# Kernel tuning notes

Measured on AMD Instinct MI355X. Metric: run time of the kernel, lower is better.

## Reference

```python
import jax, jax.numpy as jnp
import numpy as np

N_NODES = 50000
N_EDGES = 1_600_000
IN_CH = 128
HEADS = 4
OUT_CH = 16
NEG_SLOPE = 0.2


def setup_inputs() -> dict:
    key = jax.random.key(0)
    ks = jax.random.split(key, 6)
    x = jax.random.normal(ks[0], (N_NODES, IN_CH), dtype=jnp.float32)
    row = jax.random.randint(ks[1], (N_EDGES,), 0, N_NODES, dtype=jnp.int32)
    # offset in [1, N) guarantees no self loops in the input graph
    off = jax.random.randint(ks[2], (N_EDGES,), 1, N_NODES, dtype=jnp.int32)
    col = (row + off) % N_NODES
    edge_index = jnp.stack([row, col], axis=0)  # [2, E]
    edge_attr = jax.random.uniform(ks[3], (N_EDGES, HEADS), dtype=jnp.float32)
    weight = jax.random.normal(ks[4], (IN_CH, HEADS * OUT_CH), dtype=jnp.float32) * (1.0 / np.sqrt(IN_CH))
    att_weight = jax.random.normal(ks[5], (1, HEADS, 2 * OUT_CH), dtype=jnp.float32) * 0.1
    bias = jnp.zeros((HEADS * OUT_CH,), dtype=jnp.float32)
    return {"x": x, "edge_index": edge_index, "edge_attr": edge_attr,
            "weight": weight, "att_weight": att_weight, "bias": bias}


def reference(x, edge_index, edge_attr, weight, att_weight, bias):
    N = x.shape[0]
    H, C = HEADS, OUT_CH
    # linear projection: [N, in] @ [in, H*C] -> [N, H, C]
    h = (x @ weight).reshape(N, H, C)
    # add self loops (input is guaranteed self-loop free); self-loop edge_attr = 1
    loop = jnp.arange(N, dtype=edge_index.dtype)
    row = jnp.concatenate([edge_index[0], loop])
    col = jnp.concatenate([edge_index[1], loop])
    ea = jnp.concatenate([edge_attr, jnp.ones((N, H), dtype=edge_attr.dtype)], axis=0)
    edge_index_full = jnp.stack([row, col], axis=0)
    # attention score: cat([h[row], h[col]], -1) * att_weight, summed over feature dim
    a_src = att_weight[0, :, :C]   # [H, C]
    a_dst = att_weight[0, :, C:]   # [H, C]
    alpha = (jnp.einsum('ehc,hc->eh', h[row], a_src)
             + jnp.einsum('ehc,hc->eh', h[col], a_dst))  # [E+N, H]
    alpha = jnp.where(alpha >= 0, alpha, NEG_SLOPE * alpha)  # leaky_relu
    alpha = alpha * ea
    # weighted aggregation: scatter-add messages to row nodes
    msg = alpha[:, :, None] * h[col]                 # [E+N, H, C]
    out = jax.ops.segment_sum(msg, row, num_segments=N)  # [N, H, C]
    out = out.reshape(N, H * C) + bias               # concat heads
    return (out, edge_index_full, alpha)
```

## Files before the change

kernel.cpp:

```cpp
#include <hip/hip_runtime.h>

#define N_NODES 50000
#define N_EDGES 1600000
#define IN_CH 128
#define HEADS 4
#define HC 64
#define E_FULL (N_EDGES + N_NODES)
#define NEG_SLOPE 0.2f

#define BUCKET_NODES 98
#define NBUCK 512
#define BIN_TILE 2048
#define NBLK_BIN ((N_EDGES + BIN_TILE - 1) / BIN_TILE)
#define T_FLAT (NBUCK * NBLK_BIN)
#define SCANA_BLOCKS (T_FLAT / 256)

typedef __attribute__((ext_vector_type(8))) short short8v;
typedef __attribute__((ext_vector_type(4))) float float4v;

__device__ __forceinline__ float leaky(float s) { return s >= 0.f ? s : NEG_SLOPE * s; }

__device__ __forceinline__ unsigned f2bf(float f) {
    unsigned u = __float_as_uint(f);
    return (u + 0x7fffu + ((u >> 16) & 1u)) >> 16;
}
__device__ __forceinline__ float bf2f(unsigned v) {
    return __uint_as_float(v << 16);
}

__global__ __launch_bounds__(256) void wcvt_kernel(
    const float* __restrict__ w, unsigned short* __restrict__ wT)
{
    int i = blockIdx.x * 256 + threadIdx.x;
    if (i < IN_CH * HC) {
        int k = i >> 6, c = i & 63;
        wT[c * IN_CH + k] = (unsigned short)f2bf(w[i]);
    }
}

__global__ __launch_bounds__(256) void gemm_h_kernel(
    const float* __restrict__ x, const unsigned short* __restrict__ wT,
    const float* __restrict__ att, unsigned short* __restrict__ h16,
    float* __restrict__ s_src, float* __restrict__ s_dst)
{
    __shared__ unsigned short x_lds[64 * 128];
    const int tid = threadIdx.x;
    const int nbase = blockIdx.x * 64;

    #pragma unroll
    for (int s = 0; s < 8; ++s) {
        int i = s * 256 + tid;
        int node = i >> 5;
        int q = i & 31;
        float4 v = make_float4(0.f, 0.f, 0.f, 0.f);
        int gn = nbase + node;
        if (gn < N_NODES) v = ((const float4*)x)[(size_t)gn * 32 + q];
        ushort4 b;
        b.x = (unsigned short)f2bf(v.x);
        b.y = (unsigned short)f2bf(v.y);
        b.z = (unsigned short)f2bf(v.z);
        b.w = (unsigned short)f2bf(v.w);
        int chunk = q >> 1, half = q & 1;
        int sw = chunk ^ (node & 7);
        *(ushort4*)&x_lds[node * 128 + sw * 8 + half * 4] = b;
    }
    __syncthreads();

    const int wid = tid >> 6, lane = tid & 63;
    const int g = lane >> 4, m = lane & 15;
    const int rt = wid;

    float4v acc[4] = {{0.f,0.f,0.f,0.f},{0.f,0.f,0.f,0.f},
                      {0.f,0.f,0.f,0.f},{0.f,0.f,0.f,0.f}};
    #pragma unroll
    for (int kk = 0; kk < 4; ++kk) {
        int chunk = (kk * 4 + g) ^ (m & 7);
        short8v a = *(const short8v*)&x_lds[(rt * 16 + m) * 128 + chunk * 8];
        #pragma unroll
        for (int ct = 0; ct < 4; ++ct) {
            short8v bfr = *(const short8v*)&wT[(ct * 16 + m) * IN_CH + kk * 32 + g * 8];
            acc[ct] = __builtin_amdgcn_mfma_f32_16x16x32_bf16(a, bfr, acc[ct], 0, 0, 0);
        }
    }

    #pragma unroll
    for (int ct = 0; ct < 4; ++ct) {
        float as = att[ct * 32 + m];
        float ad = att[ct * 32 + 16 + m];
        float ts[4], td[4];
        #pragma unroll
        for (int r = 0; r < 4; ++r) {
            int node = nbase + rt * 16 + g * 4 + r;
            float v = acc[ct][r];
            if (node < N_NODES)
                h16[(size_t)node * HC + ct * 16 + m] = (unsigned short)f2bf(v);
            ts[r] = v * as;
            td[r] = v * ad;
        }
        #pragma unroll
        for (int msk = 1; msk <= 8; msk <<= 1) {
            #pragma unroll
            for (int r = 0; r < 4; ++r) {
                ts[r] += __shfl_xor(ts[r], msk, 64);
                td[r] += __shfl_xor(td[r], msk, 64);
            }
        }
        if (m == 0) {
            #pragma unroll
            for (int r = 0; r < 4; ++r) {
                int node = nbase + rt * 16 + g * 4 + r;
                if (node < N_NODES) {
                    s_src[node * HEADS + ct] = ts[r];
                    s_dst[node * HEADS + ct] = td[r];
                }
            }
        }
    }
}

__global__ __launch_bounds__(256) void histM_kernel(
    const int* __restrict__ ei, unsigned* __restrict__ M)
{
    __shared__ unsigned lh[NBUCK];
    const int tid = threadIdx.x;
    for (int j = tid; j < NBUCK; j += 256) lh[j] = 0;
    __syncthreads();
    const int base = blockIdx.x * BIN_TILE;
    #pragma unroll
    for (int k = 0; k < 8; ++k) {
        int e = base + k * 256 + tid;
        if (e < N_EDGES)
            atomicAdd(&lh[(unsigned)ei[e] / BUCKET_NODES], 1u);
    }
    __syncthreads();
    unsigned* Mb = M + (size_t)blockIdx.x * NBUCK;
    for (int j = tid; j < NBUCK; j += 256) Mb[j] = lh[j];
}

__device__ __forceinline__ unsigned block_excl_scan(unsigned v, unsigned* total,
                                                    int tid) {
    const int lane = tid & 63, wid = tid >> 6;
    unsigned x = v;
    #pragma unroll
    for (int d = 1; d < 64; d <<= 1) {
        unsigned t = __shfl_up(x, d, 64);
        if (lane >= d) x += t;
    }
    __shared__ unsigned wsum[4];
    if (lane == 63) wsum[wid] = x;
    __syncthreads();
    unsigned woff = 0;
    for (int i = 0; i < wid; ++i) woff += wsum[i];
    unsigned incl = x + woff;
    if (tid == 255) *total = incl;
    return incl - v;
}

__global__ __launch_bounds__(256) void scanA_kernel(
    const unsigned* __restrict__ M, unsigned* __restrict__ localx,
    unsigned* __restrict__ partials)
{
    const int tid = threadIdx.x;
    const int f = blockIdx.x * 256 + tid;
    unsigned v = 0;
    if (f < T_FLAT) {
        int bucket = f / NBLK_BIN;
        int blk = f - bucket * NBLK_BIN;
        v = M[(size_t)blk * NBUCK + bucket];
    }
    __shared__ unsigned tot;
    unsigned excl = block_excl_scan(v, &tot, tid);
    if (f < T_FLAT) localx[f] = excl;
    __syncthreads();
    if (tid == 0) partials[blockIdx.x] = tot;
}

__global__ __launch_bounds__(256) void scanB_kernel(
    const unsigned* __restrict__ partials, unsigned* __restrict__ pscan)
{
    __shared__ unsigned tot_sh;
    __shared__ unsigned carry_sh;
    const int tid = threadIdx.x;
    if (tid == 0) carry_sh = 0;
    __syncthreads();
    const int nchunk = (SCANA_BLOCKS + 255) / 256;
    for (int ch = 0; ch < nchunk; ++ch) {
        int i = ch * 256 + tid;
        unsigned v = (i < SCANA_BLOCKS) ? partials[i] : 0u;
        unsigned excl = block_excl_scan(v, &tot_sh, tid);
        unsigned carry = carry_sh;
        if (i < SCANA_BLOCKS) pscan[i] = excl + carry;
        __syncthreads();
        if (tid == 0) carry_sh += tot_sh;
        __syncthreads();
    }
}

__global__ __launch_bounds__(256) void scanC_kernel(
    const unsigned* __restrict__ localx, const unsigned* __restrict__ pscan,
    unsigned* __restrict__ S)
{
    const int f = blockIdx.x * 256 + threadIdx.x;
    if (f < T_FLAT) S[f] = localx[f] + pscan[blockIdx.x];
    if (f == 0) S[T_FLAT] = N_EDGES;
}

__global__ __launch_bounds__(256) void bin_kernel(
    const int* __restrict__ ei, const float* __restrict__ ea,
    const float* __restrict__ s_src, const float* __restrict__ s_dst,
    const unsigned* __restrict__ S, uint4* __restrict__ slots,
    float* __restrict__ alpha, float* __restrict__ eif)
{
    __shared__ unsigned lh[NBUCK];
    __shared__ unsigned lbase[NBUCK];
    const int tid = threadIdx.x;
    for (int j = tid; j < NBUCK; j += 256) lh[j] = 0;
    __syncthreads();

    const int base = blockIdx.x * BIN_TILE;
    unsigned b8[8], idx8[8], p0[8], p1[8], p2[8];
    #pragma unroll
    for (int k = 0; k < 8; ++k) {
        int e = base + k * 256 + tid;
        b8[k] = 0xffffffffu;
        if (e < N_EDGES) {
            unsigned r = (unsigned)ei[e];
            unsigned c = (unsigned)ei[N_EDGES + e];
            float4 ss = ((const float4*)s_src)[r];
            float4 sd = ((const float4*)s_dst)[c];
            float4 eav = ((const float4*)ea)[e];
            float4 a;
            a.x = leaky(ss.x + sd.x) * eav.x;
            a.y = leaky(ss.y + sd.y) * eav.y;
            a.z = leaky(ss.z + sd.z) * eav.z;
            a.w = leaky(ss.w + sd.w) * eav.w;
            ((float4*)alpha)[e] = a;
            eif[e] = (float)r;
            eif[(size_t)E_FULL + e] = (float)c;

            unsigned bk = r / BUCKET_NODES;
            unsigned rl = r - bk * BUCKET_NODES;
            b8[k] = bk;
            p0[k] = c | (rl << 16);
            p1[k] = f2bf(a.x) | (f2bf(a.y) << 16);
            p2[k] = f2bf(a.z) | (f2bf(a.w) << 16);
            idx8[k] = atomicAdd(&lh[bk], 1u);
        }
    }
    __syncthreads();
    for (int j = tid; j < NBUCK; j += 256)
        lbase[j] = S[(size_t)j * NBLK_BIN + blockIdx.x];
    __syncthreads();
    #pragma unroll
    for (int k = 0; k < 8; ++k) {
        if (b8[k] != 0xffffffffu)
            slots[lbase[b8[k]] + idx8[k]] = make_uint4(p0[k], p1[k], p2[k], 0u);
    }
}

__global__ __launch_bounds__(256) void sort_kernel(
    const unsigned* __restrict__ S, const uint4* __restrict__ slots,
    uint4* __restrict__ slots2, unsigned* __restrict__ offs)
{
    __shared__ unsigned cnt[BUCKET_NODES];
    __shared__ unsigned cur[BUCKET_NODES];
    const int b = blockIdx.x;
    const int tid = threadIdx.x;
    const unsigned start = S[(size_t)b * NBLK_BIN];
    const unsigned end   = S[(size_t)(b + 1) * NBLK_BIN];

    for (int j = tid; j < BUCKET_NODES; j += 256) cnt[j] = 0;
    __syncthreads();
    for (unsigned i = start + tid; i < end; i += 256)
        atomicAdd(&cnt[slots[i].x >> 16], 1u);
    __syncthreads();
    if (tid == 0) {
        unsigned run = 0;
        for (int j = 0; j < BUCKET_NODES; ++j) {
            unsigned c = cnt[j];
            cur[j] = run;
            run += c;
        }
    }
    __syncthreads();
    const int nstart = b * BUCKET_NODES;
    for (int j = tid; j < BUCKET_NODES; j += 256) {
        int n = nstart + j;
        if (n <= N_NODES) offs[n] = start + cur[j];
    }
    __syncthreads();
    for (unsigned i = start + tid; i < end; i += 256) {
        uint4 s = slots[i];
        unsigned rl = s.x >> 16;
        unsigned pos = start + atomicAdd(&cur[rl], 1u);
        slots2[pos] = s;
    }
}

__device__ __forceinline__ float slot_alpha(uint4 s, int hd) {
    unsigned w = (hd & 2) ? s.z : s.y;
    return bf2f((hd & 1) ? (w >> 16) : (w & 0xffffu));
}

__global__ __launch_bounds__(256) void gather_kernel(
    const unsigned short* __restrict__ h16, const float* __restrict__ s_src,
    const float* __restrict__ s_dst, const float* __restrict__ bias,
    const unsigned* __restrict__ offs, const uint4* __restrict__ slots2,
    float* __restrict__ alpha, float* __restrict__ out, float* __restrict__ eif)
{
    const int tid = threadIdx.x;
    const int n = blockIdx.x * 4 + (tid >> 6);
    if (n >= N_NODES) return;
    const int lane = tid & 63, hd = lane >> 4;

    float s_self = s_src[n * HEADS + hd] + s_dst[n * HEADS + hd];
    float acc = bias[lane] + leaky(s_self) * bf2f(h16[(size_t)n * HC + lane]);

    const unsigned start = offs[n];
    const int cnt = (int)(offs[n + 1] - start);

    int i = 0;
    for (; i + 7 < cnt; i += 8) {
        uint4 sl[8];
        float hv[8];
        #pragma unroll
        for (int u = 0; u < 8; ++u) sl[u] = slots2[start + i + u];
        #pragma unroll
        for (int u = 0; u < 8; ++u)
            hv[u] = bf2f(h16[(size_t)(sl[u].x & 0xffffu) * HC + lane]);
        #pragma unroll
        for (int u = 0; u < 8; ++u)
            acc = fmaf(slot_alpha(sl[u], hd), hv[u], acc);
    }
    for (; i < cnt; ++i) {
        uint4 s0 = slots2[start + i];
        float h0 = bf2f(h16[(size_t)(s0.x & 0xffffu) * HC + lane]);
        acc = fmaf(slot_alpha(s0, hd), h0, acc);
    }
    out[(size_t)n * HC + lane] = acc;

    if (lane < HEADS) {
        float s2 = s_src[n * HEADS + lane] + s_dst[n * HEADS + lane];
        alpha[(size_t)(N_EDGES + n) * HEADS + lane] = leaky(s2);
    }
    if (lane == 4) eif[N_EDGES + n] = (float)n;
    if (lane == 5) eif[(size_t)E_FULL + N_EDGES + n] = (float)n;
}

extern "C" void kernel_launch(void* const* d_in, const int* in_sizes, int n_in,
                              void* d_out, int out_size, void* d_ws, size_t ws_size,
                              hipStream_t stream) {
    const float* x      = (const float*)d_in[0];
    const int*   ei     = (const int*)  d_in[1];
    const float* ea     = (const float*)d_in[2];
    const float* weight = (const float*)d_in[3];
    const float* att    = (const float*)d_in[4];
    const float* bias   = (const float*)d_in[5];

    float* out   = (float*)d_out;
    float* eif   = out + (size_t)N_NODES * HC;
    float* alpha = eif + (size_t)2 * E_FULL;

    uint4* slots  = (uint4*)d_ws;
    uint4* slots2 = slots + (size_t)N_EDGES;
    unsigned short* wT = (unsigned short*)(slots2 + (size_t)N_EDGES);
    unsigned short* h16 = wT + (size_t)IN_CH * HC;
    float* s_src = (float*)(h16 + (size_t)N_NODES * HC);
    float* s_dst = s_src + (size_t)N_NODES * HEADS;
    unsigned* M        = (unsigned*)(s_dst + (size_t)N_NODES * HEADS);
    unsigned* localx   = M + (size_t)NBLK_BIN * NBUCK;
    unsigned* partials = localx + T_FLAT;
    unsigned* pscan    = partials + SCANA_BLOCKS;
    unsigned* S        = pscan + SCANA_BLOCKS;
    unsigned* offs     = S + (T_FLAT + 1);

    wcvt_kernel<<<(IN_CH * HC + 255) / 256, 256, 0, stream>>>(weight, wT);
    gemm_h_kernel<<<(N_NODES + 63) / 64, 256, 0, stream>>>(x, wT, att, h16, s_src, s_dst);
    histM_kernel<<<NBLK_BIN, 256, 0, stream>>>(ei, M);
    scanA_kernel<<<SCANA_BLOCKS, 256, 0, stream>>>(M, localx, partials);
    scanB_kernel<<<1, 256, 0, stream>>>(partials, pscan);
    scanC_kernel<<<SCANA_BLOCKS, 256, 0, stream>>>(localx, pscan, S);
    bin_kernel<<<NBLK_BIN, 256, 0, stream>>>(ei, ea, s_src, s_dst, S, slots, alpha, eif);
    sort_kernel<<<NBUCK, 256, 0, stream>>>(S, slots, slots2, offs);
    gather_kernel<<<(N_NODES + 3) / 4, 256, 0, stream>>>(
        h16, s_src, s_dst, bias, offs, slots2, alpha, out, eif);
}
```

Baseline: 167.9 us.

## Split gather into two passes by column half for L2 locality

The sort kernel now orders each node's edges by whether the source column is in the lower or upper half of the node range, and records a midpoint offset. The gather runs as two kernels: the first handles lower-half columns and the second upper-half columns, so each pass touches only half of the bf16 feature table and that half is more likely to stay in cache. The cost is an extra launch, a read-modify-write of the output between passes, a larger shared histogram, and an extra offset array.

```diff
diff --git a/kernel.cpp b/kernel.cpp
--- a/kernel.cpp
+++ b/kernel.cpp
@@ -7,6 +7,7 @@
 #define HC 64
 #define E_FULL (N_EDGES + N_NODES)
 #define NEG_SLOPE 0.2f
+#define HALF_COL 25000
 
 #define BUCKET_NODES 98
 #define NBUCK 512
@@ -260,23 +261,27 @@
 
 __global__ __launch_bounds__(256) void sort_kernel(
     const unsigned* __restrict__ S, const uint4* __restrict__ slots,
-    uint4* __restrict__ slots2, unsigned* __restrict__ offs)
-{
-    __shared__ unsigned cnt[BUCKET_NODES];
-    __shared__ unsigned cur[BUCKET_NODES];
+    uint4* __restrict__ slots2, unsigned* __restrict__ offs,
+    unsigned* __restrict__ mid)
+{
+    __shared__ unsigned cnt[BUCKET_NODES * 2];
+    __shared__ unsigned cur[BUCKET_NODES * 2];
     const int b = blockIdx.x;
     const int tid = threadIdx.x;
     const unsigned start = S[(size_t)b * NBLK_BIN];
     const unsigned end   = S[(size_t)(b + 1) * NBLK_BIN];
 
-    for (int j = tid; j < BUCKET_NODES; j += 256) cnt[j] = 0;
-    __syncthreads();
-    for (unsigned i = start + tid; i < end; i += 256)
-        atomicAdd(&cnt[slots[i].x >> 16], 1u);
+    for (int j = tid; j < BUCKET_NODES * 2; j += 256) cnt[j] = 0;
+    __syncthreads();
+    for (unsigned i = start + tid; i < end; i += 256) {
+        unsigned x0 = slots[i].x;
+        unsigned key = ((x0 >> 16) << 1) | ((x0 & 0xffffu) >= HALF_COL ? 1u : 0u);
+        atomicAdd(&cnt[key], 1u);
+    }
     __syncthreads();
     if (tid == 0) {
         unsigned run = 0;
-        for (int j = 0; j < BUCKET_NODES; ++j) {
+        for (int j = 0; j < BUCKET_NODES * 2; ++j) {
             unsigned c = cnt[j];
             cur[j] = run;
             run += c;
@@ -286,13 +291,14 @@
     const int nstart = b * BUCKET_NODES;
     for (int j = tid; j < BUCKET_NODES; j += 256) {
         int n = nstart + j;
-        if (n <= N_NODES) offs[n] = start + cur[j];
+        if (n <= N_NODES) offs[n] = start + cur[2 * j];
+        if (n < N_NODES)  mid[n]  = start + cur[2 * j + 1];
     }
     __syncthreads();
     for (unsigned i = start + tid; i < end; i += 256) {
         uint4 s = slots[i];
-        unsigned rl = s.x >> 16;
-        unsigned pos = start + atomicAdd(&cur[rl], 1u);
+        unsigned key = ((s.x >> 16) << 1) | ((s.x & 0xffffu) >= HALF_COL ? 1u : 0u);
+        unsigned pos = start + atomicAdd(&cur[key], 1u);
         slots2[pos] = s;
     }
 }
@@ -302,23 +308,11 @@
     return bf2f((hd & 1) ? (w >> 16) : (w & 0xffffu));
 }
 
-__global__ __launch_bounds__(256) void gather_kernel(
-    const unsigned short* __restrict__ h16, const float* __restrict__ s_src,
-    const float* __restrict__ s_dst, const float* __restrict__ bias,
-    const unsigned* __restrict__ offs, const uint4* __restrict__ slots2,
-    float* __restrict__ alpha, float* __restrict__ out, float* __restrict__ eif)
-{
-    const int tid = threadIdx.x;
-    const int n = blockIdx.x * 4 + (tid >> 6);
-    if (n >= N_NODES) return;
-    const int lane = tid & 63, hd = lane >> 4;
-
-    float s_self = s_src[n * HEADS + hd] + s_dst[n * HEADS + hd];
-    float acc = bias[lane] + leaky(s_self) * bf2f(h16[(size_t)n * HC + lane]);
-
-    const unsigned start = offs[n];
-    const int cnt = (int)(offs[n + 1] - start);
-
+__device__ __forceinline__ float gather_range(
+    const unsigned short* __restrict__ h16, const uint4* __restrict__ slots2,
+    unsigned start, unsigned end, int lane, int hd, float acc)
+{
+    const int cnt = (int)(end - start);
     int i = 0;
     for (; i + 7 < cnt; i += 8) {
         uint4 sl[8];
@@ -337,6 +331,40 @@
         float h0 = bf2f(h16[(size_t)(s0.x & 0xffffu) * HC + lane]);
         acc = fmaf(slot_alpha(s0, hd), h0, acc);
     }
+    return acc;
+}
+
+__global__ __launch_bounds__(256) void gatherA_kernel(
+    const unsigned short* __restrict__ h16, const float* __restrict__ s_src,
+    const float* __restrict__ s_dst, const float* __restrict__ bias,
+    const unsigned* __restrict__ offs, const unsigned* __restrict__ mid,
+    const uint4* __restrict__ slots2, float* __restrict__ out)
+{
+    const int tid = threadIdx.x;
+    const int n = blockIdx.x * 4 + (tid >> 6);
+    if (n >= N_NODES) return;
+    const int lane = tid & 63, hd = lane >> 4;
+
+    float s_self = s_src[n * HEADS + hd] + s_dst[n * HEADS + hd];
+    float acc = bias[lane] + leaky(s_self) * bf2f(h16[(size_t)n * HC + lane]);
+    acc = gather_range(h16, slots2, offs[n], mid[n], lane, hd, acc);
+    out[(size_t)n * HC + lane] = acc;
+}
+
+__global__ __launch_bounds__(256) void gatherB_kernel(
+    const unsigned short* __restrict__ h16, const float* __restrict__ s_src,
+    const float* __restrict__ s_dst,
+    const unsigned* __restrict__ offs, const unsigned* __restrict__ mid,
+    const uint4* __restrict__ slots2, float* __restrict__ alpha,
+    float* __restrict__ out, float* __restrict__ eif)
+{
+    const int tid = threadIdx.x;
+    const int n = blockIdx.x * 4 + (tid >> 6);
+    if (n >= N_NODES) return;
+    const int lane = tid & 63, hd = lane >> 4;
+
+    float acc = out[(size_t)n * HC + lane];
+    acc = gather_range(h16, slots2, mid[n], offs[n + 1], lane, hd, acc);
     out[(size_t)n * HC + lane] = acc;
 
     if (lane < HEADS) {
@@ -373,6 +401,7 @@
     unsigned* pscan    = partials + SCANA_BLOCKS;
     unsigned* S        = pscan + SCANA_BLOCKS;
     unsigned* offs     = S + (T_FLAT + 1);
+    unsigned* mid      = offs + (N_NODES + 1);
 
     wcvt_kernel<<<(IN_CH * HC + 255) / 256, 256, 0, stream>>>(weight, wT);
     gemm_h_kernel<<<(N_NODES + 63) / 64, 256, 0, stream>>>(x, wT, att, h16, s_src, s_dst);
@@ -381,7 +410,9 @@
     scanB_kernel<<<1, 256, 0, stream>>>(partials, pscan);
     scanC_kernel<<<SCANA_BLOCKS, 256, 0, stream>>>(localx, pscan, S);
     bin_kernel<<<NBLK_BIN, 256, 0, stream>>>(ei, ea, s_src, s_dst, S, slots, alpha, eif);
-    sort_kernel<<<NBUCK, 256, 0, stream>>>(S, slots, slots2, offs);
-    gather_kernel<<<(N_NODES + 3) / 4, 256, 0, stream>>>(
-        h16, s_src, s_dst, bias, offs, slots2, alpha, out, eif);
-}
+    sort_kernel<<<NBUCK, 256, 0, stream>>>(S, slots, slots2, offs, mid);
+    gatherA_kernel<<<(N_NODES + 3) / 4, 256, 0, stream>>>(
+        h16, s_src, s_dst, bias, offs, mid, slots2, out);
+    gatherB_kernel<<<(N_NODES + 3) / 4, 256, 0, stream>>>(
+        h16, s_src, s_dst, offs, mid, slots2, alpha, out, eif);
+}
```

New measurement: 185.6 us. +10.6%, slower.

## Merge GEMM with histogram launch and fold scanC into consumers

Applied to the files above, without the earlier changes.

The projection GEMM and the edge-bucket histogram become one launch, with disjoint block ranges sharing a single LDS buffer, so the two independent stages can run concurrently. The scanC kernel is removed. bin_kernel and sort_kernel now compute bucket offsets directly as localx plus pscan, which saves a launch and the write and read of the S array. The cost is a little extra index arithmetic in the consumers and higher LDS use for the histogram blocks.

```diff
diff --git a/kernel.cpp b/kernel.cpp
--- a/kernel.cpp
+++ b/kernel.cpp
@@ -12,6 +12,7 @@
 #define NBUCK 512
 #define BIN_TILE 2048
 #define NBLK_BIN ((N_EDGES + BIN_TILE - 1) / BIN_TILE)
+#define NBLK_GEMM ((N_NODES + 63) / 64)
 #define T_FLAT (NBUCK * NBLK_BIN)
 #define SCANA_BLOCKS (T_FLAT / 256)
 
@@ -38,103 +39,105 @@
     }
 }
 
-__global__ __launch_bounds__(256) void gemm_h_kernel(
+__global__ __launch_bounds__(256) void gemm_hist_kernel(
     const float* __restrict__ x, const unsigned short* __restrict__ wT,
-    const float* __restrict__ att, unsigned short* __restrict__ h16,
-    float* __restrict__ s_src, float* __restrict__ s_dst)
-{
-    __shared__ unsigned short x_lds[64 * 128];
-    const int tid = threadIdx.x;
-    const int nbase = blockIdx.x * 64;
-
-    #pragma unroll
-    for (int s = 0; s < 8; ++s) {
-        int i = s * 256 + tid;
-        int node = i >> 5;
-        int q = i & 31;
-        float4 v = make_float4(0.f, 0.f, 0.f, 0.f);
-        int gn = nbase + node;
-        if (gn < N_NODES) v = ((const float4*)x)[(size_t)gn * 32 + q];
-        ushort4 b;
-        b.x = (unsigned short)f2bf(v.x);
-        b.y = (unsigned short)f2bf(v.y);
-        b.z = (unsigned short)f2bf(v.z);
-        b.w = (unsigned short)f2bf(v.w);
-        int chunk = q >> 1, half = q & 1;
-        int sw = chunk ^ (node & 7);
-        *(ushort4*)&x_lds[node * 128 + sw * 8 + half * 4] = b;
-    }
-    __syncthreads();
-
-    const int wid = tid >> 6, lane = tid & 63;
-    const int g = lane >> 4, m = lane & 15;
-    const int rt = wid;
-
-    float4v acc[4] = {{0.f,0.f,0.f,0.f},{0.f,0.f,0.f,0.f},
-                      {0.f,0.f,0.f,0.f},{0.f,0.f,0.f,0.f}};
-    #pragma unroll
-    for (int kk = 0; kk < 4; ++kk) {
-        int chunk = (kk * 4 + g) ^ (m & 7);
-        short8v a = *(const short8v*)&x_lds[(rt * 16 + m) * 128 + chunk * 8];
+    const float* __restrict__ att, const int* __restrict__ ei,
+    unsigned short* __restrict__ h16,
+    float* __restrict__ s_src, float* __restrict__ s_dst,
+    unsigned* __restrict__ M)
+{
+    __shared__ __align__(16) unsigned char smem[64 * 128 * 2];
+    const int tid = threadIdx.x;
+
+    if (blockIdx.x < NBLK_GEMM) {
+        unsigned short* x_lds = (unsigned short*)smem;
+        const int nbase = blockIdx.x * 64;
+
+        #pragma unroll
+        for (int s = 0; s < 8; ++s) {
+            int i = s * 256 + tid;
+            int node = i >> 5;
+            int q = i & 31;
+            float4 v = make_float4(0.f, 0.f, 0.f, 0.f);
+            int gn = nbase + node;
+            if (gn < N_NODES) v = ((const float4*)x)[(size_t)gn * 32 + q];
+            ushort4 b;
+            b.x = (unsigned short)f2bf(v.x);
+            b.y = (unsigned short)f2bf(v.y);
+            b.z = (unsigned short)f2bf(v.z);
+            b.w = (unsigned short)f2bf(v.w);
+            int chunk = q >> 1, half = q & 1;
+            int sw = chunk ^ (node & 7);
+            *(ushort4*)&x_lds[node * 128 + sw * 8 + half * 4] = b;
+        }
+        __syncthreads();
+
+        const int wid = tid >> 6, lane = tid & 63;
+        const int g = lane >> 4, m = lane & 15;
+        const int rt = wid;
+
+        float4v acc[4] = {{0.f,0.f,0.f,0.f},{0.f,0.f,0.f,0.f},
+                          {0.f,0.f,0.f,0.f},{0.f,0.f,0.f,0.f}};
+        #pragma unroll
+        for (int kk = 0; kk < 4; ++kk) {
+            int chunk = (kk * 4 + g) ^ (m & 7);
+            short8v a = *(const short8v*)&x_lds[(rt * 16 + m) * 128 + chunk * 8];
+            #pragma unroll
+            for (int ct = 0; ct < 4; ++ct) {
+                short8v bfr = *(const short8v*)&wT[(ct * 16 + m) * IN_CH + kk * 32 + g * 8];
+                acc[ct] = __builtin_amdgcn_mfma_f32_16x16x32_bf16(a, bfr, acc[ct], 0, 0, 0);
+            }
+        }
+
         #pragma unroll
         for (int ct = 0; ct < 4; ++ct) {
-            short8v bfr = *(const short8v*)&wT[(ct * 16 + m) * IN_CH + kk * 32 + g * 8];
-            acc[ct] = __builtin_amdgcn_mfma_f32_16x16x32_bf16(a, bfr, acc[ct], 0, 0, 0);
-        }
-    }
-
-    #pragma unroll
-    for (int ct = 0; ct < 4; ++ct) {
-        float as = att[ct * 32 + m];
-        float ad = att[ct * 32 + 16 + m];
-        float ts[4], td[4];
-        #pragma unroll
-        for (int r = 0; r < 4; ++r) {
-            int node = nbase + rt * 16 + g * 4 + r;
-            float v = acc[ct][r];
-            if (node < N_NODES)
-                h16[(size_t)node * HC + ct * 16 + m] = (unsigned short)f2bf(v);
-            ts[r] = v * as;
-            td[r] = v * ad;
-        }
-        #pragma unroll
-        for (int msk = 1; msk <= 8; msk <<= 1) {
-            #pragma unroll
-            for (int r = 0; r < 4; ++r) {
-                ts[r] += __shfl_xor(ts[r], msk, 64);
-                td[r] += __shfl_xor(td[r], msk, 64);
-            }
-        }
-        if (m == 0) {
+            float as = att[ct * 32 + m];
+            float ad = att[ct * 32 + 16 + m];
+            float ts[4], td[4];
             #pragma unroll
             for (int r = 0; r < 4; ++r) {
                 int node = nbase + rt * 16 + g * 4 + r;
-                if (node < N_NODES) {
-                    s_src[node * HEADS + ct] = ts[r];
-                    s_dst[node * HEADS + ct] = td[r];
+                float v = acc[ct][r];
+                if (node < N_NODES)
+                    h16[(size_t)node * HC + ct * 16 + m] = (unsigned short)f2bf(v);
+                ts[r] = v * as;
+                td[r] = v * ad;
+            }
+            #pragma unroll
+            for (int msk = 1; msk <= 8; msk <<= 1) {
+                #pragma unroll
+                for (int r = 0; r < 4; ++r) {
+                    ts[r] += __shfl_xor(ts[r], msk, 64);
+                    td[r] += __shfl_xor(td[r], msk, 64);
                 }
             }
-        }
-    }
-}
-
-__global__ __launch_bounds__(256) void histM_kernel(
-    const int* __restrict__ ei, unsigned* __restrict__ M)
-{
-    __shared__ unsigned lh[NBUCK];
-    const int tid = threadIdx.x;
-    for (int j = tid; j < NBUCK; j += 256) lh[j] = 0;
-    __syncthreads();
-    const int base = blockIdx.x * BIN_TILE;
-    #pragma unroll
-    for (int k = 0; k < 8; ++k) {
-        int e = base + k * 256 + tid;
-        if (e < N_EDGES)
-            atomicAdd(&lh[(unsigned)ei[e] / BUCKET_NODES], 1u);
-    }
-    __syncthreads();
-    unsigned* Mb = M + (size_t)blockIdx.x * NBUCK;
-    for (int j = tid; j < NBUCK; j += 256) Mb[j] = lh[j];
+            if (m == 0) {
+                #pragma unroll
+                for (int r = 0; r < 4; ++r) {
+                    int node = nbase + rt * 16 + g * 4 + r;
+                    if (node < N_NODES) {
+                        s_src[node * HEADS + ct] = ts[r];
+                        s_dst[node * HEADS + ct] = td[r];
+                    }
+                }
+            }
+        }
+    } else {
+        unsigned* lh = (unsigned*)smem;
+        const int bid = blockIdx.x - NBLK_GEMM;
+        for (int j = tid; j < NBUCK; j += 256) lh[j] = 0;
+        __syncthreads();
+        const int base = bid * BIN_TILE;
+        #pragma unroll
+        for (int k = 0; k < 8; ++k) {
+            int e = base + k * 256 + tid;
+            if (e < N_EDGES)
+                atomicAdd(&lh[(unsigned)ei[e] / BUCKET_NODES], 1u);
+        }
+        __syncthreads();
+        unsigned* Mb = M + (size_t)bid * NBUCK;
+        for (int j = tid; j < NBUCK; j += 256) Mb[j] = lh[j];
+    }
 }
 
 __device__ __forceinline__ unsigned block_excl_scan(unsigned v, unsigned* total,
@@ -196,20 +199,19 @@
     }
 }
 
-__global__ __launch_bounds__(256) void scanC_kernel(
-    const unsigned* __restrict__ localx, const unsigned* __restrict__ pscan,
-    unsigned* __restrict__ S)
-{
-    const int f = blockIdx.x * 256 + threadIdx.x;
-    if (f < T_FLAT) S[f] = localx[f] + pscan[blockIdx.x];
-    if (f == 0) S[T_FLAT] = N_EDGES;
+__device__ __forceinline__ unsigned S_at(const unsigned* __restrict__ localx,
+                                         const unsigned* __restrict__ pscan,
+                                         unsigned f) {
+    return (f >= (unsigned)T_FLAT) ? (unsigned)N_EDGES
+                                   : localx[f] + pscan[f >> 8];
 }
 
 __global__ __launch_bounds__(256) void bin_kernel(
     const int* __restrict__ ei, const float* __restrict__ ea,
     const float* __restrict__ s_src, const float* __restrict__ s_dst,
-    const unsigned* __restrict__ S, uint4* __restrict__ slots,
-    float* __restrict__ alpha, float* __restrict__ eif)
+    const unsigned* __restrict__ localx, const unsigned* __restrict__ pscan,
+    uint4* __restrict__ slots, float* __restrict__ alpha,
+    float* __restrict__ eif)
 {
     __shared__ unsigned lh[NBUCK];
     __shared__ unsigned lbase[NBUCK];
@@ -248,8 +250,10 @@
         }
     }
     __syncthreads();
-    for (int j = tid; j < NBUCK; j += 256)
-        lbase[j] = S[(size_t)j * NBLK_BIN + blockIdx.x];
+    for (int j = tid; j < NBUCK; j += 256) {
+        unsigned f = (unsigned)j * NBLK_BIN + blockIdx.x;
+        lbase[j] = localx[f] + pscan[f >> 8];
+    }
     __syncthreads();
     #pragma unroll
     for (int k = 0; k < 8; ++k) {
@@ -259,15 +263,16 @@
 }
 
 __global__ __launch_bounds__(256) void sort_kernel(
-    const unsigned* __restrict__ S, const uint4* __restrict__ slots,
-    uint4* __restrict__ slots2, unsigned* __restrict__ offs)
+    const unsigned* __restrict__ localx, const unsigned* __restrict__ pscan,
+    const uint4* __restrict__ slots, uint4* __restrict__ slots2,
+    unsigned* __restrict__ offs)
 {
     __shared__ unsigned cnt[BUCKET_NODES];
     __shared__ unsigned cur[BUCKET_NODES];
     const int b = blockIdx.x;
     const int tid = threadIdx.x;
-    const unsigned start = S[(size_t)b * NBLK_BIN];
-    const unsigned end   = S[(size_t)(b + 1) * NBLK_BIN];
+    const unsigned start = S_at(localx, pscan, (unsigned)b * NBLK_BIN);
+    const unsigned end   = S_at(localx, pscan, (unsigned)(b + 1) * NBLK_BIN);
 
     for (int j = tid; j < BUCKET_NODES; j += 256) cnt[j] = 0;
     __syncthreads();
@@ -371,17 +376,16 @@
     unsigned* localx   = M + (size_t)NBLK_BIN * NBUCK;
     unsigned* partials = localx + T_FLAT;
     unsigned* pscan    = partials + SCANA_BLOCKS;
-    unsigned* S        = pscan + SCANA_BLOCKS;
-    unsigned* offs     = S + (T_FLAT + 1);
+    unsigned* offs     = pscan + SCANA_BLOCKS;
 
     wcvt_kernel<<<(IN_CH * HC + 255) / 256, 256, 0, stream>>>(weight, wT);
-    gemm_h_kernel<<<(N_NODES + 63) / 64, 256, 0, stream>>>(x, wT, att, h16, s_src, s_dst);
-    histM_kernel<<<NBLK_BIN, 256, 0, stream>>>(ei, M);
+    gemm_hist_kernel<<<NBLK_GEMM + NBLK_BIN, 256, 0, stream>>>(
+        x, wT, att, ei, h16, s_src, s_dst, M);
     scanA_kernel<<<SCANA_BLOCKS, 256, 0, stream>>>(M, localx, partials);
     scanB_kernel<<<1, 256, 0, stream>>>(partials, pscan);
-    scanC_kernel<<<SCANA_BLOCKS, 256, 0, stream>>>(localx, pscan, S);
-    bin_kernel<<<NBLK_BIN, 256, 0, stream>>>(ei, ea, s_src, s_dst, S, slots, alpha, eif);
-    sort_kernel<<<NBUCK, 256, 0, stream>>>(S, slots, slots2, offs);
+    bin_kernel<<<NBLK_BIN, 256, 0, stream>>>(
+        ei, ea, s_src, s_dst, localx, pscan, slots, alpha, eif);
+    sort_kernel<<<NBUCK, 256, 0, stream>>>(localx, pscan, slots, slots2, offs);
     gather_kernel<<<(N_NODES + 3) / 4, 256, 0, stream>>>(
         h16, s_src, s_dst, bias, offs, slots2, alpha, out, eif);
 }
```

Measured after the change: 161.6 us. 1.04x faster.
